# Kernel optimization log

Measured on AMD Instinct MI355X. Metric: run time of the kernel, lower is better.

## Reference

```python
import jax, jax.numpy as jnp
import numpy as np

T_STEPS = 30
HIDDEN = 16
INPUT_DIM = 32
OUTPUT_DIM = 1
BATCH = 262144


def setup_inputs() -> dict:
    key = jax.random.key(0)
    ks = jax.random.split(key, 8)
    u = lambda k, shape: jax.random.uniform(k, shape, jnp.float32, -0.25, 0.25)
    return {
        "x": jax.random.normal(ks[0], (BATCH, INPUT_DIM), jnp.float32),
        "T": T_STEPS,
        "W_ih": u(ks[1], (HIDDEN, INPUT_DIM)),
        "W_hh": u(ks[2], (HIDDEN, HIDDEN)),
        "b_ih": u(ks[3], (HIDDEN,)),
        "b_hh": u(ks[4], (HIDDEN,)),
        "W_fc": jax.random.normal(ks[5], (OUTPUT_DIM, HIDDEN), jnp.float32) * 0.25,
        "b_fc": jax.random.normal(ks[6], (OUTPUT_DIM,), jnp.float32) * 0.25,
    }


def reference(x, T, W_ih, W_hh, b_ih, b_hh, W_fc, b_fc):
    # Input is the same at every timestep (x repeated T times), so the
    # input projection is computed once and reused across the scan.
    xproj = x @ W_ih.T + b_ih + b_hh  # [B, H]
    h0 = jnp.zeros((x.shape[0], W_hh.shape[0]), dtype=x.dtype)

    def step(h, _):
        h = jnp.tanh(xproj + h @ W_hh.T)  # Elman: tanh(Wx+b_ih + Uh+b_hh)
        return h, h

    _, hs = jax.lax.scan(step, h0, None, length=T)  # [T, B, H]
    hs = jnp.transpose(hs, (1, 0, 2))               # [B, T, H] (batch_first)
    return hs @ W_fc.T + b_fc                       # [B, T, output_dim]
```

## Files before the change

### kernel.cpp

```cpp
#include <hip/hip_runtime.h>


#define T_STEPS 30
#define BLOCK   256
#define SCALE   2.8853900817779268f

typedef _Float16 v4h __attribute__((ext_vector_type(4)));
typedef __fp16   v2fp __attribute__((ext_vector_type(2)));
typedef float    v4f __attribute__((ext_vector_type(4)));

struct h4 { v2fp lo, hi; };

__device__ __forceinline__ float tanh_pre(float a) {
    float e = __builtin_amdgcn_exp2f(a);
    float r = __builtin_amdgcn_rcpf(1.0f + e);
    return fmaf(-2.0f, r, 1.0f);
}

__global__ __launch_bounds__(BLOCK, 8) void rnn_mfma(
    const float* __restrict__ x,
    const float* __restrict__ W_ih,
    const float* __restrict__ W_hh,
    const float* __restrict__ b_ih,
    const float* __restrict__ b_hh,
    const float* __restrict__ W_fc,
    const float* __restrict__ b_fc,
    float* __restrict__ out)
{
    __shared__ float tmp[64 * T_STEPS];

    const int tid  = threadIdx.x;
    const int w    = tid >> 6;
    const int lane = tid & 63;
    const int r    = lane & 15;
    const int q    = lane >> 4;
    const int j0   = 4 * q;

    const size_t row = (size_t)blockIdx.x * 64 + (size_t)w * 16 + r;

    float a0 = b_ih[j0 + 0] + b_hh[j0 + 0];
    float a1 = b_ih[j0 + 1] + b_hh[j0 + 1];
    float a2 = b_ih[j0 + 2] + b_hh[j0 + 2];
    float a3 = b_ih[j0 + 3] + b_hh[j0 + 3];
    {
        const float4* xrow = (const float4*)(x + row * 32);
#pragma unroll
        for (int c4 = 0; c4 < 8; ++c4) {
            float4 xv = xrow[c4];
            const float4 w0 = *(const float4*)(W_ih + (j0 + 0) * 32 + c4 * 4);
            const float4 w1 = *(const float4*)(W_ih + (j0 + 1) * 32 + c4 * 4);
            const float4 w2 = *(const float4*)(W_ih + (j0 + 2) * 32 + c4 * 4);
            const float4 w3 = *(const float4*)(W_ih + (j0 + 3) * 32 + c4 * 4);
            a0 = fmaf(w0.x, xv.x, fmaf(w0.y, xv.y, fmaf(w0.z, xv.z, fmaf(w0.w, xv.w, a0))));
            a1 = fmaf(w1.x, xv.x, fmaf(w1.y, xv.y, fmaf(w1.z, xv.z, fmaf(w1.w, xv.w, a1))));
            a2 = fmaf(w2.x, xv.x, fmaf(w2.y, xv.y, fmaf(w2.z, xv.z, fmaf(w2.w, xv.w, a2))));
            a3 = fmaf(w3.x, xv.x, fmaf(w3.y, xv.y, fmaf(w3.z, xv.z, fmaf(w3.w, xv.w, a3))));
        }
    }
    const v4f xpv = {a0 * SCALE, a1 * SCALE, a2 * SCALE, a3 * SCALE};

    v4h whh;
    {
        float4 wr = *(const float4*)(W_hh + r * 16 + 4 * q);
        whh[0] = (_Float16)(wr.x * SCALE);
        whh[1] = (_Float16)(wr.y * SCALE);
        whh[2] = (_Float16)(wr.z * SCALE);
        whh[3] = (_Float16)(wr.w * SCALE);
    }

    v4h afc;
#pragma unroll
    for (int i = 0; i < 4; ++i) {
        float wv = W_fc[4 * q + i];
        _Float16 hi = (_Float16)wv;
        _Float16 lo = (_Float16)(wv - (float)hi);
        afc[i] = (r == 0) ? hi : ((r == 1) ? lo : (_Float16)0.0f);
    }
    const float bfc = b_fc[0];
    const v4f zfc = {(q == 0) ? bfc : 0.0f, 0.0f, 0.0f, 0.0f};

    v4h s = {(_Float16)0.0f, (_Float16)0.0f, (_Float16)0.0f, (_Float16)0.0f};

    float* myout = &tmp[(w * 16 + r) * T_STEPS];

#pragma unroll
    for (int t = 0; t < T_STEPS; ++t) {
        v4f acc = __builtin_amdgcn_mfma_f32_16x16x16f16(whh, s, xpv, 0, 0, 0);

        float h0 = tanh_pre(acc[0]);
        float h1 = tanh_pre(acc[1]);
        float h2 = tanh_pre(acc[2]);
        float h3 = tanh_pre(acc[3]);

        h4 p;
        p.lo = __builtin_amdgcn_cvt_pkrtz(h0, h1);
        p.hi = __builtin_amdgcn_cvt_pkrtz(h2, h3);
        s = __builtin_bit_cast(v4h, p);

        v4f f = __builtin_amdgcn_mfma_f32_16x16x16f16(afc, s, zfc, 0, 0, 0);

        if (lane < 16)
            myout[t] = f[0] + f[1];
    }

    __syncthreads();

    float* oblk = out + (size_t)blockIdx.x * (64 * T_STEPS);
    for (int idx = tid; idx < 64 * T_STEPS; idx += BLOCK)
        oblk[idx] = tmp[idx];
}

extern "C" void kernel_launch(void* const* d_in, const int* in_sizes, int n_in,
                              void* d_out, int out_size, void* d_ws, size_t ws_size,
                              hipStream_t stream) {
    const float* x    = (const float*)d_in[0];
    const float* W_ih = (const float*)d_in[2];
    const float* W_hh = (const float*)d_in[3];
    const float* b_ih = (const float*)d_in[4];
    const float* b_hh = (const float*)d_in[5];
    const float* W_fc = (const float*)d_in[6];
    const float* b_fc = (const float*)d_in[7];
    float* out = (float*)d_out;

    const int B = in_sizes[0] / 32;
    const int grid = B / 64;

    rnn_mfma<<<grid, BLOCK, 0, stream>>>(x, W_ih, W_hh, b_ih, b_hh, W_fc, b_fc, out);
}
```

Before: 131.2 us.

## Interleave two independent recurrence chains per wave and replace rcp with Newton iteration

Each wave now handles 32 rows as two independent 16-row MFMA recurrence chains, so the MFMA and tanh latencies of one chain can overlap with the other. The grid is halved and LDS staging doubled. The tanh reciprocal switches from hardware rcp to a bit-trick initial guess refined by two Newton steps, with the input clamped via fmed3. The output copy loop is fully unrolled. This trades more registers and possibly lower occupancy for more instruction-level parallelism.

```diff
diff --git a/kernel.cpp b/kernel.cpp
--- a/kernel.cpp
+++ b/kernel.cpp
@@ -12,8 +12,12 @@
 struct h4 { v2fp lo, hi; };
 
 __device__ __forceinline__ float tanh_pre(float a) {
-    float e = __builtin_amdgcn_exp2f(a);
-    float r = __builtin_amdgcn_rcpf(1.0f + e);
+    float ac = __builtin_amdgcn_fmed3f(a, 14.0f, -14.0f);
+    float e  = __builtin_amdgcn_exp2f(ac);
+    float d  = 1.0f + e;
+    float r  = __uint_as_float(0x7EF311C3u - __float_as_uint(d));
+    r = r * fmaf(-d, r, 2.0f);
+    r = r * fmaf(-d, r, 2.0f);
     return fmaf(-2.0f, r, 1.0f);
 }
 
@@ -27,7 +31,7 @@
     const float* __restrict__ b_fc,
     float* __restrict__ out)
 {
-    __shared__ float tmp[64 * T_STEPS];
+    __shared__ float tmp[128 * T_STEPS];
 
     const int tid  = threadIdx.x;
     const int w    = tid >> 6;
@@ -36,28 +40,37 @@
     const int q    = lane >> 4;
     const int j0   = 4 * q;
 
-    const size_t row = (size_t)blockIdx.x * 64 + (size_t)w * 16 + r;
+    const size_t rowA = (size_t)blockIdx.x * 128 + (size_t)w * 32 + r;
+    const size_t rowB = rowA + 16;
 
     float a0 = b_ih[j0 + 0] + b_hh[j0 + 0];
     float a1 = b_ih[j0 + 1] + b_hh[j0 + 1];
     float a2 = b_ih[j0 + 2] + b_hh[j0 + 2];
     float a3 = b_ih[j0 + 3] + b_hh[j0 + 3];
+    float c0 = a0, c1 = a1, c2 = a2, c3 = a3;
     {
-        const float4* xrow = (const float4*)(x + row * 32);
+        const float4* xA = (const float4*)(x + rowA * 32);
+        const float4* xB = (const float4*)(x + rowB * 32);
 #pragma unroll
         for (int c4 = 0; c4 < 8; ++c4) {
-            float4 xv = xrow[c4];
+            float4 xa = xA[c4];
+            float4 xb = xB[c4];
             const float4 w0 = *(const float4*)(W_ih + (j0 + 0) * 32 + c4 * 4);
             const float4 w1 = *(const float4*)(W_ih + (j0 + 1) * 32 + c4 * 4);
             const float4 w2 = *(const float4*)(W_ih + (j0 + 2) * 32 + c4 * 4);
             const float4 w3 = *(const float4*)(W_ih + (j0 + 3) * 32 + c4 * 4);
-            a0 = fmaf(w0.x, xv.x, fmaf(w0.y, xv.y, fmaf(w0.z, xv.z, fmaf(w0.w, xv.w, a0))));
-            a1 = fmaf(w1.x, xv.x, fmaf(w1.y, xv.y, fmaf(w1.z, xv.z, fmaf(w1.w, xv.w, a1))));
-            a2 = fmaf(w2.x, xv.x, fmaf(w2.y, xv.y, fmaf(w2.z, xv.z, fmaf(w2.w, xv.w, a2))));
-            a3 = fmaf(w3.x, xv.x, fmaf(w3.y, xv.y, fmaf(w3.z, xv.z, fmaf(w3.w, xv.w, a3))));
+            a0 = fmaf(w0.x, xa.x, fmaf(w0.y, xa.y, fmaf(w0.z, xa.z, fmaf(w0.w, xa.w, a0))));
+            a1 = fmaf(w1.x, xa.x, fmaf(w1.y, xa.y, fmaf(w1.z, xa.z, fmaf(w1.w, xa.w, a1))));
+            a2 = fmaf(w2.x, xa.x, fmaf(w2.y, xa.y, fmaf(w2.z, xa.z, fmaf(w2.w, xa.w, a2))));
+            a3 = fmaf(w3.x, xa.x, fmaf(w3.y, xa.y, fmaf(w3.z, xa.z, fmaf(w3.w, xa.w, a3))));
+            c0 = fmaf(w0.x, xb.x, fmaf(w0.y, xb.y, fmaf(w0.z, xb.z, fmaf(w0.w, xb.w, c0))));
+            c1 = fmaf(w1.x, xb.x, fmaf(w1.y, xb.y, fmaf(w1.z, xb.z, fmaf(w1.w, xb.w, c1))));
+            c2 = fmaf(w2.x, xb.x, fmaf(w2.y, xb.y, fmaf(w2.z, xb.z, fmaf(w2.w, xb.w, c2))));
+            c3 = fmaf(w3.x, xb.x, fmaf(w3.y, xb.y, fmaf(w3.z, xb.z, fmaf(w3.w, xb.w, c3))));
         }
     }
-    const v4f xpv = {a0 * SCALE, a1 * SCALE, a2 * SCALE, a3 * SCALE};
+    const v4f xpA = {a0 * SCALE, a1 * SCALE, a2 * SCALE, a3 * SCALE};
+    const v4f xpB = {c0 * SCALE, c1 * SCALE, c2 * SCALE, c3 * SCALE};
 
     v4h whh;
     {
@@ -79,35 +92,51 @@
     const float bfc = b_fc[0];
     const v4f zfc = {(q == 0) ? bfc : 0.0f, 0.0f, 0.0f, 0.0f};
 
-    v4h s = {(_Float16)0.0f, (_Float16)0.0f, (_Float16)0.0f, (_Float16)0.0f};
+    v4h sA = {(_Float16)0.0f, (_Float16)0.0f, (_Float16)0.0f, (_Float16)0.0f};
+    v4h sB = sA;
 
-    float* myout = &tmp[(w * 16 + r) * T_STEPS];
+    float* outA = &tmp[(w * 32 + r) * T_STEPS];
+    float* outB = outA + 16 * T_STEPS;
 
 #pragma unroll
     for (int t = 0; t < T_STEPS; ++t) {
-        v4f acc = __builtin_amdgcn_mfma_f32_16x16x16f16(whh, s, xpv, 0, 0, 0);
+        v4f accA = __builtin_amdgcn_mfma_f32_16x16x16f16(whh, sA, xpA, 0, 0, 0);
+        v4f accB = __builtin_amdgcn_mfma_f32_16x16x16f16(whh, sB, xpB, 0, 0, 0);
 
-        float h0 = tanh_pre(acc[0]);
-        float h1 = tanh_pre(acc[1]);
-        float h2 = tanh_pre(acc[2]);
-        float h3 = tanh_pre(acc[3]);
+        float hA0 = tanh_pre(accA[0]);
+        float hB0 = tanh_pre(accB[0]);
+        float hA1 = tanh_pre(accA[1]);
+        float hB1 = tanh_pre(accB[1]);
+        float hA2 = tanh_pre(accA[2]);
+        float hB2 = tanh_pre(accB[2]);
+        float hA3 = tanh_pre(accA[3]);
+        float hB3 = tanh_pre(accB[3]);
 
-        h4 p;
-        p.lo = __builtin_amdgcn_cvt_pkrtz(h0, h1);
-        p.hi = __builtin_amdgcn_cvt_pkrtz(h2, h3);
-        s = __builtin_bit_cast(v4h, p);
+        h4 pA, pB;
+        pA.lo = __builtin_amdgcn_cvt_pkrtz(hA0, hA1);
+        pA.hi = __builtin_amdgcn_cvt_pkrtz(hA2, hA3);
+        pB.lo = __builtin_amdgcn_cvt_pkrtz(hB0, hB1);
+        pB.hi = __builtin_amdgcn_cvt_pkrtz(hB2, hB3);
+        sA = __builtin_bit_cast(v4h, pA);
+        sB = __builtin_bit_cast(v4h, pB);
 
-        v4f f = __builtin_amdgcn_mfma_f32_16x16x16f16(afc, s, zfc, 0, 0, 0);
+        v4f fA = __builtin_amdgcn_mfma_f32_16x16x16f16(afc, sA, zfc, 0, 0, 0);
+        v4f fB = __builtin_amdgcn_mfma_f32_16x16x16f16(afc, sB, zfc, 0, 0, 0);
 
-        if (lane < 16)
-            myout[t] = f[0] + f[1];
+        if (lane < 16) {
+            outA[t] = fA[0] + fA[1];
+            outB[t] = fB[0] + fB[1];
+        }
     }
 
     __syncthreads();
 
-    float* oblk = out + (size_t)blockIdx.x * (64 * T_STEPS);
-    for (int idx = tid; idx < 64 * T_STEPS; idx += BLOCK)
+    float* oblk = out + (size_t)blockIdx.x * (128 * T_STEPS);
+#pragma unroll
+    for (int k = 0; k < (128 * T_STEPS) / BLOCK; ++k) {
+        int idx = tid + k * BLOCK;
         oblk[idx] = tmp[idx];
+    }
 }
 
 extern "C" void kernel_launch(void* const* d_in, const int* in_sizes, int n_in,
@@ -123,7 +152,7 @@
     float* out = (float*)d_out;
 
     const int B = in_sizes[0] / 32;
-    const int grid = B / 64;
+    const int grid = B / 128;
 
     rnn_mfma<<<grid, BLOCK, 0, stream>>>(x, W_ih, W_hh, b_ih, b_hh, W_fc, b_fc, out);
 }
```

Result: slower. 142.5 us (+8.6%).
